# Optimization experiments

Hardware: AMD Instinct MI355X
Metric: run time of the kernel (lower is better)

Reference implementation:

```python
import jax, jax.numpy as jnp
import numpy as np

N = 10000      # nodes
E = 160000     # edges (avg degree 16)
D = 128        # channels
H = 4          # heads
C = 128        # per-head dim (PyG: out_channels per head = channels)
HC = H * C
EPS_SOFTMAX = 1e-16
EPS_NORM = 1e-5


def setup_inputs() -> dict:
    key = jax.random.key(0)
    ks = jax.random.split(key, 12)
    s = 1.0 / np.sqrt(D)
    sb = 1.0 / np.sqrt(3 * D)
    return {
        "x": jax.random.normal(ks[0], (N, D), jnp.float32),
        "edge_index": jax.random.randint(ks[1], (2, E), 0, N, dtype=jnp.int64),
        "Wq": jax.random.normal(ks[2], (D, HC), jnp.float32) * s,
        "bq": jnp.zeros((HC,), jnp.float32),
        "Wk": jax.random.normal(ks[3], (D, HC), jnp.float32) * s,
        "bk": jnp.zeros((HC,), jnp.float32),
        "Wv": jax.random.normal(ks[4], (D, HC), jnp.float32) * s,
        "bv": jnp.zeros((HC,), jnp.float32),
        "Wskip": jax.random.normal(ks[5], (D, D), jnp.float32) * s,
        "bskip": jnp.zeros((D,), jnp.float32),
        "Wbeta": jax.random.normal(ks[6], (3 * D,), jnp.float32) * sb,  # lin_beta, bias=False
        "gn_weight": jnp.ones((D,), jnp.float32),
        "gn_bias": jnp.zeros((D,), jnp.float32),
        "gn_mean_scale": jnp.ones((D,), jnp.float32),
    }


def reference(x, edge_index, Wq, bq, Wk, bk, Wv, bv, Wskip, bskip, Wbeta,
              gn_weight, gn_bias, gn_mean_scale):
    n = x.shape[0]
    src, dst = edge_index[0], edge_index[1]  # messages flow src(j) -> dst(i)

    # Projections [N,H,C]
    q = (x @ Wq + bq).reshape(n, H, C)
    k = (x @ Wk + bk).reshape(n, H, C)
    v = (x @ Wv + bv).reshape(n, H, C)

    # Per-edge attention logits [E,H]
    alpha = jnp.einsum('ehc,ehc->eh', q[dst], k[src]) / jnp.sqrt(jnp.float32(C))

    # Segment softmax over incoming edges of each dst node
    amax = jax.ops.segment_max(alpha, dst, num_segments=n)       # [N,H]
    amax = jnp.where(jnp.isfinite(amax), amax, 0.0)
    ex = jnp.exp(alpha - amax[dst])                              # [E,H]
    denom = jax.ops.segment_sum(ex, dst, num_segments=n)         # [N,H]
    attn = ex / (denom[dst] + EPS_SOFTMAX)                       # [E,H]

    # Weighted scatter-aggregate, then mean over heads (concat=False)
    msgs = attn[:, :, None] * v[src]                             # [E,H,C]
    out = jax.ops.segment_sum(msgs, dst, num_segments=n)         # [N,H,C]
    out = out.mean(axis=1)                                       # [N,D]

    # Beta-gated skip (PyG: beta = sigmoid(lin_beta([out, x_r, out - x_r])))
    skip = x @ Wskip + bskip
    beta = jax.nn.sigmoid(jnp.concatenate([out, skip, out - skip], axis=-1) @ Wbeta)
    beta = beta[:, None]
    out = beta * skip + (1.0 - beta) * out

    # GraphNorm (single graph): (x - mean_scale*mean) / sqrt(var + eps) * w + b
    mean = out.mean(axis=0)
    centered = out - gn_mean_scale * mean
    var = (centered * centered).mean(axis=0)
    out = gn_weight * centered / jnp.sqrt(var + EPS_NORM) + gn_bias

    # GELU (exact) + residual (shapes match); dropout is identity in eval
    out = jax.nn.gelu(out, approximate=False)
    return out + x
```

## Files before the change

kernel.cpp:

```cpp
#include <hip/hip_runtime.h>
#include <hip/hip_bf16.h>
#include <math.h>

#define D_DIM 128
#define HC_DIM 512
#define CAP 128

typedef __attribute__((ext_vector_type(8))) short bf16x8;
typedef __attribute__((ext_vector_type(4))) float f32x4;
typedef __attribute__((ext_vector_type(2))) float f32x2;
typedef __attribute__((ext_vector_type(2))) _Float16 h16x2;

static __device__ __forceinline__ unsigned short f2bf(float f) {
  unsigned u = __float_as_uint(f);
  unsigned r = (u + 0x7fffu + ((u >> 16) & 1u)) >> 16;
  return (unsigned short)r;
}
static __device__ __forceinline__ float bflo(unsigned u) {
  return __uint_as_float(u << 16);
}
static __device__ __forceinline__ float bfhi(unsigned u) {
  return __uint_as_float(u & 0xffff0000u);
}

__global__ void prep_kernel(const float* __restrict__ x,
                            const float* __restrict__ Wq, const float* __restrict__ Wk,
                            const float* __restrict__ Wv, const float* __restrict__ Wskip,
                            const float* __restrict__ bq, const float* __restrict__ bk,
                            const float* __restrict__ bv, const float* __restrict__ bskip,
                            unsigned short* __restrict__ xb,
                            unsigned short* __restrict__ wcat,
                            float* __restrict__ bcat,
                            int* __restrict__ zbase, int zwords, int N) {
  int t = blockIdx.x * 256 + threadIdx.x;
  int X4 = N * 32;
  if (t < X4) {
    float4 f = *(const float4*)&x[t * 4];
    ushort4 o;
    o.x = f2bf(f.x); o.y = f2bf(f.y); o.z = f2bf(f.z); o.w = f2bf(f.w);
    *(ushort4*)&xb[t * 4] = o;
  } else if (t < X4 + 1664 * 128) {
    int widx = t - X4;
    if (widx < 3 * 65536) {
      int segi = widx >> 16;
      int r = widx & 65535;
      int kk = r >> 9;
      int m = r & 511;
      const float* W = (segi == 0) ? Wq : (segi == 1) ? Wk : Wv;
      wcat[(size_t)(segi * 512 + m) * 128 + kk] = f2bf(W[kk * 512 + m]);
    } else {
      int r = widx - 3 * 65536;
      int kk = r >> 7;
      int m = r & 127;
      wcat[(size_t)(1536 + m) * 128 + kk] = f2bf(Wskip[kk * 128 + m]);
    }
  } else if (t < X4 + 1664 * 128 + 1664) {
    int b = t - X4 - 1664 * 128;
    bcat[b] = (b < 512) ? bq[b] : (b < 1024) ? bk[b - 512]
            : (b < 1536) ? bv[b - 1024] : bskip[b - 1536];
  } else if (t < X4 + 1664 * 128 + 1664 + zwords) {
    zbase[t - X4 - 1664 * 128 - 1664] = 0;
  }
}

__global__ __launch_bounds__(256) void gemm_mfma_kernel(
    const unsigned short* __restrict__ Xb, const unsigned short* __restrict__ Wt,
    const float* __restrict__ bcat, unsigned short* __restrict__ qb,
    unsigned short* __restrict__ kf, unsigned char* __restrict__ v8,
    float* __restrict__ skip,
    const int* __restrict__ src, const int* __restrict__ dst,
    int* __restrict__ cnt, int* __restrict__ bsrc, int N, int E) {
  const int tid = threadIdx.x;
  {
    int nblk = gridDim.x;
    int lb = blockIdx.x;
    int per = (E + nblk - 1) / nblk;
    int e0 = lb * per;
    int e1 = min(e0 + per, E);
    for (int e = e0 + tid; e < e1; e += 256) {
      int d = dst[e];
      int p = atomicAdd(&cnt[d], 1);
      if (p < CAP) bsrc[d * CAP + p] = src[e];
    }
  }
  const int L = blockIdx.x;
  const int xcd = L & 7;
  const int m = L >> 3;
  const int slab = (m / 26) * 8 + xcd;
  const int ctile = m % 26;

  const int wave = tid >> 6, lane = tid & 63;
  const int l16 = lane & 15, quad = lane >> 4;
  const int row0 = (slab * 4 + wave) * 64;
  const int col0 = ctile * 64;

  const unsigned short* xrow[4];
#pragma unroll
  for (int i = 0; i < 4; ++i) {
    int r = row0 + i * 16 + l16;
    if (r >= N) r = N - 1;
    xrow[i] = Xb + (size_t)r * 128;
  }
  const unsigned short* wrow[4];
  float bias[4];
#pragma unroll
  for (int j = 0; j < 4; ++j) {
    int c = col0 + j * 16 + l16;
    wrow[j] = Wt + (size_t)c * 128;
    bias[j] = bcat[c];
  }

  f32x4 acc[4][4] = {};
#pragma unroll
  for (int kk = 0; kk < 4; ++kk) {
    int k0 = kk * 32 + quad * 8;
    bf16x8 a[4], b[4];
#pragma unroll
    for (int i = 0; i < 4; ++i) a[i] = *(const bf16x8*)(xrow[i] + k0);
#pragma unroll
    for (int j = 0; j < 4; ++j) b[j] = *(const bf16x8*)(wrow[j] + k0);
#pragma unroll
    for (int i = 0; i < 4; ++i)
#pragma unroll
      for (int j = 0; j < 4; ++j)
        acc[i][j] = __builtin_amdgcn_mfma_f32_16x16x32_bf16(a[i], b[j], acc[i][j], 0, 0, 0);
  }

  const int kind = (col0 < 512) ? 0 : (col0 < 1024) ? 1 : (col0 < 1536) ? 2 : 3;
#pragma unroll
  for (int i = 0; i < 4; ++i) {
#pragma unroll
    for (int reg = 0; reg < 4; ++reg) {
      int r = row0 + i * 16 + quad * 4 + reg;
      if (r < N) {
#pragma unroll
        for (int j = 0; j < 4; ++j) {
          int cidx = col0 + j * 16 + l16;
          float val = acc[i][j][reg] + bias[j];
          if (kind == 0) {
            qb[(size_t)r * 512 + cidx] = f2bf(val);
          } else if (kind == 1) {
            _Float16 hv = (_Float16)val;
            kf[(size_t)r * 512 + cidx - 512] = *(unsigned short*)&hv;
          } else if (kind == 2) {
            int pk = __builtin_amdgcn_cvt_pk_fp8_f32(val, val, 0, false);
            v8[(size_t)r * 512 + cidx - 1024] = (unsigned char)pk;
          } else {
            skip[(size_t)r * 128 + cidx - 1536] = val;
          }
        }
      }
    }
  }
}

__global__ __launch_bounds__(256) void attn_kernel(
    const unsigned short* __restrict__ qb, const unsigned short* __restrict__ kf,
    const unsigned char* __restrict__ v8, const int* __restrict__ cnt,
    const int* __restrict__ bsrc, unsigned* __restrict__ oh, int N, int nper) {
  int bx = blockIdx.x;
  int head = bx / nper;
  int tid = threadIdx.x;
  int w = tid >> 6, lane = tid & 63;
  int node = (bx - head * nper) * 4 + w;
  if (node >= N) return;
  int g = lane >> 4, j = lane & 15;

  const float qscale = 0.08838834764831845f * 1.4426950408889634f;
  int4 qi = *(const int4*)(qb + (size_t)node * 512 + head * 128 + j * 8);
  h16x2 qh0, qh1, qh2, qh3;
  qh0[0] = (_Float16)(bflo(qi.x) * qscale); qh0[1] = (_Float16)(bfhi(qi.x) * qscale);
  qh1[0] = (_Float16)(bflo(qi.y) * qscale); qh1[1] = (_Float16)(bfhi(qi.y) * qscale);
  qh2[0] = (_Float16)(bflo(qi.z) * qscale); qh2[1] = (_Float16)(bfhi(qi.z) * qscale);
  qh3[0] = (_Float16)(bflo(qi.w) * qscale); qh3[1] = (_Float16)(bfhi(qi.w) * qscale);

  const unsigned short* kb = kf + head * 128 + j * 8;
  const unsigned char* vb = v8 + head * 128 + j * 8;
  int count = min(cnt[node], CAP);
  const int* bp = bsrc + node * CAP;
  float lsum = 0.f;
  float o0 = 0.f, o1 = 0.f, o2 = 0.f, o3 = 0.f;
  float o4 = 0.f, o5 = 0.f, o6 = 0.f, o7 = 0.f;

  if (count > 0) {
    int e = bp[(g < count) ? g : 0];
    uint4 kw = *(const uint4*)(kb + (size_t)e * 512);
    uint2 vw = *(const uint2*)(vb + (size_t)e * 512);
    for (int idx = 0; idx < count; idx += 4) {
      int rem = count - idx;
      int nrem = rem - 4;
      int en = (nrem > 0) ? bp[idx + 4 + ((g < nrem) ? g : 0)] : e;
      uint4 kwn = *(const uint4*)(kb + (size_t)en * 512);
      uint2 vwn = *(const uint2*)(vb + (size_t)en * 512);
      float p = __builtin_amdgcn_fdot2(qh0, *(h16x2*)&kw.x, 0.f, false);
      p = __builtin_amdgcn_fdot2(qh1, *(h16x2*)&kw.y, p, false);
      p = __builtin_amdgcn_fdot2(qh2, *(h16x2*)&kw.z, p, false);
      p = __builtin_amdgcn_fdot2(qh3, *(h16x2*)&kw.w, p, false);
      p += __shfl_xor(p, 1);
      p += __shfl_xor(p, 2);
      p += __shfl_xor(p, 4);
      p += __shfl_xor(p, 8);
      float a = (g < rem) ? p : -1e30f;
      float wgt = exp2f(a);
      f32x2 v01 = __builtin_amdgcn_cvt_pk_f32_fp8(vw.x, false);
      f32x2 v23 = __builtin_amdgcn_cvt_pk_f32_fp8(vw.x, true);
      f32x2 v45 = __builtin_amdgcn_cvt_pk_f32_fp8(vw.y, false);
      f32x2 v67 = __builtin_amdgcn_cvt_pk_f32_fp8(vw.y, true);
      lsum += wgt;
      o0 += wgt * v01.x; o1 += wgt * v01.y;
      o2 += wgt * v23.x; o3 += wgt * v23.y;
      o4 += wgt * v45.x; o5 += wgt * v45.y;
      o6 += wgt * v67.x; o7 += wgt * v67.y;
      kw = kwn; vw = vwn; e = en;
    }
  }
  o0 += __shfl_xor(o0, 16); o0 += __shfl_xor(o0, 32);
  o1 += __shfl_xor(o1, 16); o1 += __shfl_xor(o1, 32);
  o2 += __shfl_xor(o2, 16); o2 += __shfl_xor(o2, 32);
  o3 += __shfl_xor(o3, 16); o3 += __shfl_xor(o3, 32);
  o4 += __shfl_xor(o4, 16); o4 += __shfl_xor(o4, 32);
  o5 += __shfl_xor(o5, 16); o5 += __shfl_xor(o5, 32);
  o6 += __shfl_xor(o6, 16); o6 += __shfl_xor(o6, 32);
  o7 += __shfl_xor(o7, 16); o7 += __shfl_xor(o7, 32);
  lsum += __shfl_xor(lsum, 16); lsum += __shfl_xor(lsum, 32);
  float inv = 1.f / (lsum + 1e-16f);
  if (g == 0) {
    unsigned d0 = (unsigned)f2bf(o0 * inv) | ((unsigned)f2bf(o1 * inv) << 16);
    unsigned d1 = (unsigned)f2bf(o2 * inv) | ((unsigned)f2bf(o3 * inv) << 16);
    unsigned d2 = (unsigned)f2bf(o4 * inv) | ((unsigned)f2bf(o5 * inv) << 16);
    unsigned d3 = (unsigned)f2bf(o6 * inv) | ((unsigned)f2bf(o7 * inv) << 16);
    int4 st; st.x = (int)d0; st.y = (int)d1; st.z = (int)d2; st.w = (int)d3;
    *(int4*)(oh + ((size_t)head * N + node) * 64 + j * 4) = st;
  }
}

__global__ __launch_bounds__(256) void combine_kernel(
    const unsigned* __restrict__ oh, const float* __restrict__ skip,
    const float* __restrict__ Wbeta, float* __restrict__ out2,
    float* __restrict__ colsum, float* __restrict__ colsq, int N) {
  int tid = threadIdx.x;
  int lane = tid & 63, w = tid >> 6;
  int wid = blockIdx.x * 4 + w;
  float2 wb0 = *(const float2*)&Wbeta[lane * 2];
  float2 wb1 = *(const float2*)&Wbeta[128 + lane * 2];
  float2 wb2 = *(const float2*)&Wbeta[256 + lane * 2];
  float cs0 = 0.f, cq0 = 0.f, cs1 = 0.f, cq1 = 0.f;
#pragma unroll
  for (int k = 0; k < 4; ++k) {
    int n = wid + k * 2500;
    if (n < N) {
      unsigned h0 = oh[((size_t)0 * N + n) * 64 + lane];
      unsigned h1 = oh[((size_t)1 * N + n) * 64 + lane];
      unsigned h2 = oh[((size_t)2 * N + n) * 64 + lane];
      unsigned h3 = oh[((size_t)3 * N + n) * 64 + lane];
      float a0 = 0.25f * (bflo(h0) + bflo(h1) + bflo(h2) + bflo(h3));
      float a1 = 0.25f * (bfhi(h0) + bfhi(h1) + bfhi(h2) + bfhi(h3));
      float2 s = *(const float2*)&skip[(size_t)n * 128 + lane * 2];
      float p = a0 * wb0.x + s.x * wb1.x + (a0 - s.x) * wb2.x +
                a1 * wb0.y + s.y * wb1.y + (a1 - s.y) * wb2.y;
#pragma unroll
      for (int dmask = 1; dmask < 64; dmask <<= 1) p += __shfl_xor(p, dmask);
      float beta = 1.f / (1.f + __expf(-p));
      float o0 = beta * s.x + (1.f - beta) * a0;
      float o1 = beta * s.y + (1.f - beta) * a1;
      float2 ov; ov.x = o0; ov.y = o1;
      *(float2*)&out2[(size_t)n * 128 + lane * 2] = ov;
      cs0 += o0; cq0 += o0 * o0;
      cs1 += o1; cq1 += o1 * o1;
    }
  }
  __shared__ float red[4][128];
  __shared__ float redq[4][128];
  red[w][lane * 2] = cs0;
  red[w][lane * 2 + 1] = cs1;
  redq[w][lane * 2] = cq0;
  redq[w][lane * 2 + 1] = cq1;
  __syncthreads();
  if (w == 0) {
    int c = lane * 2;
    float s0 = red[0][c] + red[1][c] + red[2][c] + red[3][c];
    float s1 = red[0][c + 1] + red[1][c + 1] + red[2][c + 1] + red[3][c + 1];
    float q0 = redq[0][c] + redq[1][c] + redq[2][c] + redq[3][c];
    float q1 = redq[0][c + 1] + redq[1][c + 1] + redq[2][c + 1] + redq[3][c + 1];
    atomicAdd(&colsum[c], s0);
    atomicAdd(&colsum[c + 1], s1);
    atomicAdd(&colsq[c], q0);
    atomicAdd(&colsq[c + 1], q1);
  }
}

__global__ void final_kernel(const float* __restrict__ out2,
                             const float* __restrict__ colsum,
                             const float* __restrict__ colsq,
                             const float* __restrict__ gnw,
                             const float* __restrict__ gnb,
                             const float* __restrict__ gnms,
                             const float* __restrict__ x,
                             float* __restrict__ y, int total2, float invN) {
  int i = blockIdx.x * 256 + threadIdx.x;
  if (i < total2) {
    int c = (i & 63) * 2;
    float2 cs = *(const float2*)&colsum[c];
    float2 cq = *(const float2*)&colsq[c];
    float2 gw = *(const float2*)&gnw[c];
    float2 gb = *(const float2*)&gnb[c];
    float2 gs = *(const float2*)&gnms[c];
    float mean0 = cs.x * invN, mean1 = cs.y * invN;
    float var0 = cq.x * invN - mean0 * mean0 * gs.x * (2.f - gs.x);
    float var1 = cq.y * invN - mean1 * mean1 * gs.y * (2.f - gs.y);
    float mul0 = gw.x / sqrtf(var0 + 1e-5f);
    float mul1 = gw.y / sqrtf(var1 + 1e-5f);
    float2 o = *(const float2*)&out2[i * 2];
    float2 xx = *(const float2*)&x[i * 2];
    float t0 = (o.x - gs.x * mean0) * mul0 + gb.x;
    float t1 = (o.y - gs.y * mean1) * mul1 + gb.y;
    float g0 = 0.5f * t0 * (1.f + erff(t0 * 0.70710678118654752f));
    float g1 = 0.5f * t1 * (1.f + erff(t1 * 0.70710678118654752f));
    float2 r; r.x = g0 + xx.x; r.y = g1 + xx.y;
    *(float2*)&y[i * 2] = r;
  }
}

extern "C" void kernel_launch(void* const* d_in, const int* in_sizes, int n_in,
                              void* d_out, int out_size, void* d_ws, size_t ws_size,
                              hipStream_t stream) {
  const float* x     = (const float*)d_in[0];
  const int*   ei    = (const int*)d_in[1];
  const float* Wq    = (const float*)d_in[2];
  const float* bq    = (const float*)d_in[3];
  const float* Wk    = (const float*)d_in[4];
  const float* bk    = (const float*)d_in[5];
  const float* Wv    = (const float*)d_in[6];
  const float* bv    = (const float*)d_in[7];
  const float* Wskip = (const float*)d_in[8];
  const float* bskip = (const float*)d_in[9];
  const float* Wbeta = (const float*)d_in[10];
  const float* gnw   = (const float*)d_in[11];
  const float* gnb   = (const float*)d_in[12];
  const float* gnms  = (const float*)d_in[13];

  const int N = in_sizes[0] / D_DIM;
  const int E = in_sizes[1] / 2;
  const int* src = ei;
  const int* dst = ei + E;

  char* p = (char*)d_ws;
  unsigned short* qb = (unsigned short*)p; p += (size_t)N * 512 * 2;
  unsigned short* kf = (unsigned short*)p; p += (size_t)N * 512 * 2;
  unsigned char*  v8 = (unsigned char*)p;  p += (size_t)N * 512;
  unsigned*       oh = (unsigned*)p;       p += (size_t)4 * N * 64 * 4;
  float*          skip = (float*)p;        p += (size_t)N * 128 * 4;
  float*          out2 = (float*)p;        p += (size_t)N * 128 * 4;
  int*   cnt    = (int*)p;   p += (size_t)N * 4;
  float* colsum = (float*)p; p += 128 * 4;
  float* colsq  = (float*)p; p += 128 * 4;
  int zwords = N + 256;
  int* bsrc   = (int*)p;   p += (size_t)N * CAP * 4;
  unsigned short* wcat = (unsigned short*)p; p += (size_t)1664 * 128 * 2;
  float* bcat = (float*)p; p += 1664 * 4;
  unsigned short* xb = (unsigned short*)oh;

  int prepTotal = N * 32 + 1664 * 128 + 1664 + zwords;
  prep_kernel<<<(prepTotal + 255) / 256, 256, 0, stream>>>(
      x, Wq, Wk, Wv, Wskip, bq, bk, bv, bskip, xb, wcat, bcat, cnt, zwords, N);

  gemm_mfma_kernel<<<1040, 256, 0, stream>>>(
      xb, wcat, bcat, qb, kf, v8, skip, src, dst, cnt, bsrc, N, E);

  int nper = (N + 3) / 4;
  attn_kernel<<<nper * 4, 256, 0, stream>>>(qb, kf, v8, cnt, bsrc, oh, N, nper);

  combine_kernel<<<625, 256, 0, stream>>>(oh, skip, Wbeta, out2, colsum, colsq, N);

  int total2 = N * D_DIM / 2;
  final_kernel<<<(total2 + 255) / 256, 256, 0, stream>>>(
      out2, colsum, colsq, gnw, gnb, gnms, x, (float*)d_out, total2, 1.f / (float)N);
}
```

Baseline: 195.0 us.

## Fuse head-mean and beta-gated skip into attention kernel, one node per block

After: 194.4 us. Within noise of the previous version (-0.3%).

```diff
diff --git a/kernel.cpp b/kernel.cpp
--- a/kernel.cpp
+++ b/kernel.cpp
@@ -157,25 +157,23 @@
 __global__ __launch_bounds__(256) void attn_kernel(
     const unsigned short* __restrict__ qb, const unsigned short* __restrict__ kf,
     const unsigned char* __restrict__ v8, const int* __restrict__ cnt,
-    const int* __restrict__ bsrc, unsigned* __restrict__ oh, int N, int nper) {
-  int bx = blockIdx.x;
-  int head = bx / nper;
+    const int* __restrict__ bsrc, const float* __restrict__ skip,
+    const float* __restrict__ Wbeta, float* __restrict__ out2, int N) {
+  int node = blockIdx.x;
   int tid = threadIdx.x;
   int w = tid >> 6, lane = tid & 63;
-  int node = (bx - head * nper) * 4 + w;
-  if (node >= N) return;
   int g = lane >> 4, j = lane & 15;
 
   const float qscale = 0.08838834764831845f * 1.4426950408889634f;
-  int4 qi = *(const int4*)(qb + (size_t)node * 512 + head * 128 + j * 8);
+  int4 qi = *(const int4*)(qb + (size_t)node * 512 + w * 128 + j * 8);
   h16x2 qh0, qh1, qh2, qh3;
   qh0[0] = (_Float16)(bflo(qi.x) * qscale); qh0[1] = (_Float16)(bfhi(qi.x) * qscale);
   qh1[0] = (_Float16)(bflo(qi.y) * qscale); qh1[1] = (_Float16)(bfhi(qi.y) * qscale);
   qh2[0] = (_Float16)(bflo(qi.z) * qscale); qh2[1] = (_Float16)(bfhi(qi.z) * qscale);
   qh3[0] = (_Float16)(bflo(qi.w) * qscale); qh3[1] = (_Float16)(bfhi(qi.w) * qscale);
 
-  const unsigned short* kb = kf + head * 128 + j * 8;
-  const unsigned char* vb = v8 + head * 128 + j * 8;
+  const unsigned short* kb = kf + w * 128 + j * 8;
+  const unsigned char* vb = v8 + w * 128 + j * 8;
   int count = min(cnt[node], CAP);
   const int* bp = bsrc + node * CAP;
   float lsum = 0.f;
@@ -224,49 +222,49 @@
   o7 += __shfl_xor(o7, 16); o7 += __shfl_xor(o7, 32);
   lsum += __shfl_xor(lsum, 16); lsum += __shfl_xor(lsum, 32);
   float inv = 1.f / (lsum + 1e-16f);
+
+  __shared__ float ohs[4][128];
   if (g == 0) {
-    unsigned d0 = (unsigned)f2bf(o0 * inv) | ((unsigned)f2bf(o1 * inv) << 16);
-    unsigned d1 = (unsigned)f2bf(o2 * inv) | ((unsigned)f2bf(o3 * inv) << 16);
-    unsigned d2 = (unsigned)f2bf(o4 * inv) | ((unsigned)f2bf(o5 * inv) << 16);
-    unsigned d3 = (unsigned)f2bf(o6 * inv) | ((unsigned)f2bf(o7 * inv) << 16);
-    int4 st; st.x = (int)d0; st.y = (int)d1; st.z = (int)d2; st.w = (int)d3;
-    *(int4*)(oh + ((size_t)head * N + node) * 64 + j * 4) = st;
-  }
-}
-
-__global__ __launch_bounds__(256) void combine_kernel(
-    const unsigned* __restrict__ oh, const float* __restrict__ skip,
-    const float* __restrict__ Wbeta, float* __restrict__ out2,
-    float* __restrict__ colsum, float* __restrict__ colsq, int N) {
+    float4 s0; s0.x = o0 * inv; s0.y = o1 * inv; s0.z = o2 * inv; s0.w = o3 * inv;
+    float4 s1; s1.x = o4 * inv; s1.y = o5 * inv; s1.z = o6 * inv; s1.w = o7 * inv;
+    *(float4*)&ohs[w][j * 8] = s0;
+    *(float4*)&ohs[w][j * 8 + 4] = s1;
+  }
+  __syncthreads();
+  if (w == 0) {
+    int c = lane * 2;
+    float a0 = 0.25f * (ohs[0][c] + ohs[1][c] + ohs[2][c] + ohs[3][c]);
+    float a1 = 0.25f * (ohs[0][c + 1] + ohs[1][c + 1] + ohs[2][c + 1] + ohs[3][c + 1]);
+    float2 s = *(const float2*)&skip[(size_t)node * 128 + c];
+    float2 wb0 = *(const float2*)&Wbeta[c];
+    float2 wb1 = *(const float2*)&Wbeta[128 + c];
+    float2 wb2 = *(const float2*)&Wbeta[256 + c];
+    float p = a0 * wb0.x + s.x * wb1.x + (a0 - s.x) * wb2.x +
+              a1 * wb0.y + s.y * wb1.y + (a1 - s.y) * wb2.y;
+#pragma unroll
+    for (int dmask = 1; dmask < 64; dmask <<= 1) p += __shfl_xor(p, dmask);
+    float beta = 1.f / (1.f + __expf(-p));
+    float2 ov;
+    ov.x = beta * s.x + (1.f - beta) * a0;
+    ov.y = beta * s.y + (1.f - beta) * a1;
+    *(float2*)&out2[(size_t)node * 128 + c] = ov;
+  }
+}
+
+__global__ __launch_bounds__(256) void colstat_kernel(
+    const float* __restrict__ out2, float* __restrict__ colsum,
+    float* __restrict__ colsq, int N) {
   int tid = threadIdx.x;
   int lane = tid & 63, w = tid >> 6;
   int wid = blockIdx.x * 4 + w;
-  float2 wb0 = *(const float2*)&Wbeta[lane * 2];
-  float2 wb1 = *(const float2*)&Wbeta[128 + lane * 2];
-  float2 wb2 = *(const float2*)&Wbeta[256 + lane * 2];
   float cs0 = 0.f, cq0 = 0.f, cs1 = 0.f, cq1 = 0.f;
 #pragma unroll
   for (int k = 0; k < 4; ++k) {
     int n = wid + k * 2500;
     if (n < N) {
-      unsigned h0 = oh[((size_t)0 * N + n) * 64 + lane];
-      unsigned h1 = oh[((size_t)1 * N + n) * 64 + lane];
-      unsigned h2 = oh[((size_t)2 * N + n) * 64 + lane];
-      unsigned h3 = oh[((size_t)3 * N + n) * 64 + lane];
-      float a0 = 0.25f * (bflo(h0) + bflo(h1) + bflo(h2) + bflo(h3));
-      float a1 = 0.25f * (bfhi(h0) + bfhi(h1) + bfhi(h2) + bfhi(h3));
-      float2 s = *(const float2*)&skip[(size_t)n * 128 + lane * 2];
-      float p = a0 * wb0.x + s.x * wb1.x + (a0 - s.x) * wb2.x +
-                a1 * wb0.y + s.y * wb1.y + (a1 - s.y) * wb2.y;
-#pragma unroll
-      for (int dmask = 1; dmask < 64; dmask <<= 1) p += __shfl_xor(p, dmask);
-      float beta = 1.f / (1.f + __expf(-p));
-      float o0 = beta * s.x + (1.f - beta) * a0;
-      float o1 = beta * s.y + (1.f - beta) * a1;
-      float2 ov; ov.x = o0; ov.y = o1;
-      *(float2*)&out2[(size_t)n * 128 + lane * 2] = ov;
-      cs0 += o0; cq0 += o0 * o0;
-      cs1 += o1; cq1 += o1 * o1;
+      float2 o = *(const float2*)&out2[(size_t)n * 128 + lane * 2];
+      cs0 += o.x; cq0 += o.x * o.x;
+      cs1 += o.y; cq1 += o.y * o.y;
     }
   }
   __shared__ float red[4][128];
@@ -348,7 +346,6 @@
   unsigned short* qb = (unsigned short*)p; p += (size_t)N * 512 * 2;
   unsigned short* kf = (unsigned short*)p; p += (size_t)N * 512 * 2;
   unsigned char*  v8 = (unsigned char*)p;  p += (size_t)N * 512;
-  unsigned*       oh = (unsigned*)p;       p += (size_t)4 * N * 64 * 4;
   float*          skip = (float*)p;        p += (size_t)N * 128 * 4;
   float*          out2 = (float*)p;        p += (size_t)N * 128 * 4;
   int*   cnt    = (int*)p;   p += (size_t)N * 4;
@@ -358,7 +355,7 @@
   int* bsrc   = (int*)p;   p += (size_t)N * CAP * 4;
   unsigned short* wcat = (unsigned short*)p; p += (size_t)1664 * 128 * 2;
   float* bcat = (float*)p; p += 1664 * 4;
-  unsigned short* xb = (unsigned short*)oh;
+  unsigned short* xb = (unsigned short*)out2;
 
   int prepTotal = N * 32 + 1664 * 128 + 1664 + zwords;
   prep_kernel<<<(prepTotal + 255) / 256, 256, 0, stream>>>(
@@ -367,10 +364,9 @@
   gemm_mfma_kernel<<<1040, 256, 0, stream>>>(
       xb, wcat, bcat, qb, kf, v8, skip, src, dst, cnt, bsrc, N, E);
 
-  int nper = (N + 3) / 4;
-  attn_kernel<<<nper * 4, 256, 0, stream>>>(qb, kf, v8, cnt, bsrc, oh, N, nper);
-
-  combine_kernel<<<625, 256, 0, stream>>>(oh, skip, Wbeta, out2, colsum, colsq, N);
+  attn_kernel<<<N, 256, 0, stream>>>(qb, kf, v8, cnt, bsrc, skip, Wbeta, out2, N);
+
+  colstat_kernel<<<625, 256, 0, stream>>>(out2, colsum, colsq, N);
 
   int total2 = N * D_DIM / 2;
   final_kernel<<<(total2 + 255) / 256, 256, 0, stream>>>(
```
